# Performance work log

Measured on AMD Instinct MI355X. Metric: run time of the kernel, lower is better.

The kernel has to match this reference:

```python
import jax, jax.numpy as jnp
import numpy as np

IN_CH = 12
STEP = 4
UPLAG = 2048
HIDDEN = 1024
OUTPUT = 256
BATCH = 2048
FEAT = UPLAG // STEP  # per-channel conv output length


def setup_inputs() -> dict:
    key = jax.random.key(0)
    ks = jax.random.split(key, 7)
    s = 1.0 / np.sqrt(STEP)
    x = jax.random.normal(ks[0], (BATCH, IN_CH, UPLAG), dtype=jnp.float32)
    # per-channel Conv1d(1,1,step,step) weights/biases, stacked: [C, step], [C]
    W1 = jax.random.uniform(ks[1], (IN_CH, STEP), jnp.float32, -s, s)
    b1 = jax.random.uniform(ks[2], (IN_CH,), jnp.float32, -s, s)
    d_in = IN_CH * FEAT
    s2 = 1.0 / np.sqrt(d_in)
    W2 = jax.random.uniform(ks[3], (d_in, HIDDEN), jnp.float32, -s2, s2)
    b2 = jax.random.uniform(ks[4], (HIDDEN,), jnp.float32, -s2, s2)
    s3 = 1.0 / np.sqrt(HIDDEN)
    W3 = jax.random.uniform(ks[5], (HIDDEN, OUTPUT), jnp.float32, -s3, s3)
    b3 = jax.random.uniform(ks[6], (OUTPUT,), jnp.float32, -s3, s3)
    return {"x": x, "W1": W1, "b1": b1, "W2": W2, "b2": b2, "W3": W3, "b3": b3}


def reference(x, W1, b1, W2, b2, W3, b3):
    B, C, L = x.shape
    # Non-overlapping patch reduction equivalent to Conv1d(1,1,step,step) per channel:
    # view [B, C, F, step], contract step dim against per-channel kernel.
    xp = x.reshape(B, C, L // STEP, STEP)
    conv = jnp.einsum('bcfk,ck->bcf', xp, W1) + b1[None, :, None]  # [B, C, F]
    flat = conv.reshape(B, C * (L // STEP))  # concat order: channel-major, matches torch.cat
    h = jax.nn.relu(flat @ W2 + b2)
    out = h @ W3 + b3
    return out.reshape(B, 1, -1)
```

## Files before the change

kernel.cpp:

```cpp
#include <hip/hip_runtime.h>
#include <hip/hip_bf16.h>

#define BATCH   2048
#define IN_CH   12
#define UPLAG   2048
#define STEP    4
#define FEAT    512
#define DIN     6144
#define HIDDEN  1024
#define OUTPUT  256

typedef __bf16 bf16x8 __attribute__((ext_vector_type(8)));
typedef float  f32x4  __attribute__((ext_vector_type(4)));

__device__ __forceinline__ unsigned short f2bf(float f) {
  unsigned int u = __builtin_bit_cast(unsigned int, f);
  unsigned int r = (u + 0x7fffu + ((u >> 16) & 1u)) >> 16;
  return (unsigned short)r;
}

__device__ __forceinline__ float bf2f(unsigned short h) {
  unsigned int u = ((unsigned int)h) << 16;
  return __builtin_bit_cast(float, u);
}

__device__ __forceinline__ void async_copy16(const unsigned short* g, unsigned short* l) {
  __builtin_amdgcn_global_load_lds(
      (const __attribute__((address_space(1))) unsigned int*)g,
      (__attribute__((address_space(3))) unsigned int*)l, 16, 0, 0);
}

#define CONV_BLOCKS 4096
#define W2T_BLOCKS  1536
#define W3T_BLOCKS  64

__global__ __launch_bounds__(256) void prep_kernel(
    const float* __restrict__ x, const float* __restrict__ W1,
    const float* __restrict__ b1, unsigned short* __restrict__ flatA,
    const float* __restrict__ W2, unsigned short* __restrict__ W2T,
    const float* __restrict__ W3, unsigned short* __restrict__ W3T)
{
  __shared__ float tile[64][65];
  const int t = threadIdx.x;
  int b = blockIdx.x;

  if (b < CONV_BLOCKS) {
    const int total = BATCH * DIN;
    for (int gid = b * 256 + t; gid < total; gid += CONV_BLOCKS * 256) {
      int cf = gid % DIN;
      int c  = cf >> 9;
      float4 xv = ((const float4*)x)[gid];
      float4 wv = ((const float4*)W1)[c];
      float v = xv.x * wv.x + xv.y * wv.y + xv.z * wv.z + xv.w * wv.w + b1[c];
      flatA[gid] = f2bf(v);
    }
    return;
  }

  const float* in; unsigned short* outp; int R, Ncol, bx, by;
  if (b < CONV_BLOCKS + W2T_BLOCKS) {
    int idx = b - CONV_BLOCKS;
    in = W2; outp = W2T; R = DIN; Ncol = HIDDEN;
    bx = (idx & 15) * 64; by = (idx >> 4) * 64;
  } else {
    int idx = b - CONV_BLOCKS - W2T_BLOCKS;
    in = W3; outp = W3T; R = HIDDEN; Ncol = OUTPUT;
    bx = (idx & 3) * 64; by = (idx >> 2) * 64;
  }
  int tx = t & 63, ty = t >> 6;
  #pragma unroll
  for (int i = 0; i < 64; i += 4)
    tile[ty + i][tx] = in[(size_t)(by + ty + i) * Ncol + bx + tx];
  __syncthreads();
  #pragma unroll
  for (int i = 0; i < 64; i += 4)
    outp[(size_t)(bx + ty + i) * R + by + tx] = f2bf(tile[tx][ty + i]);
}

#define G1_BM 128
#define G1_BN 128
#define G1_BK 64
#define SPLITK 6

__global__ __launch_bounds__(256, 2) void gemm1_kernel(
    const unsigned short* __restrict__ A,
    const unsigned short* __restrict__ BT,
    unsigned short* __restrict__ Cp,
    int M, int N, int K)
{
  __shared__ unsigned short As[G1_BM * G1_BK];
  __shared__ unsigned short Bs[G1_BN * G1_BK];
  const int t    = threadIdx.x;
  const int lane = t & 63;
  const int wave = t >> 6;

  int b    = blockIdx.x;
  int xcdg = b & 7;
  int rest = b >> 3;
  int xt   = rest & 7;
  int zz   = rest >> 3;
  int zt   = zz >> 1;
  int yt   = (xcdg << 1) | (zz & 1);

  const int m0 = yt * G1_BM;
  const int n0 = xt * G1_BN;
  const int Ks = K / SPLITK;
  const int kbeg = zt * Ks;

  const int wm = (wave >> 1) * 64;
  const int wn = (wave & 1) * 64;
  const int lm = lane & 15;
  const int kgrp = lane >> 4;

  f32x4 acc[4][4];
  #pragma unroll
  for (int i = 0; i < 4; i++)
    #pragma unroll
    for (int j = 0; j < 4; j++) {
      f32x4 z = {0.f, 0.f, 0.f, 0.f};
      acc[i][j] = z;
    }

  const unsigned short* Ag = A  + (size_t)m0 * K + kbeg;
  const unsigned short* Bg = BT + (size_t)n0 * K + kbeg;

  for (int kk = 0; kk < Ks; kk += G1_BK) {
    #pragma unroll
    for (int r = 0; r < 4; ++r) {
      int c = r * 256 + t;
      int row = c >> 3;
      int gk  = (c & 7) ^ (row & 7);
      async_copy16(Ag + (size_t)row * K + kk + gk * 8, As + c * 8);
    }
    #pragma unroll
    for (int r = 0; r < 4; ++r) {
      int c = r * 256 + t;
      int row = c >> 3;
      int gk  = (c & 7) ^ (row & 7);
      async_copy16(Bg + (size_t)row * K + kk + gk * 8, Bs + c * 8);
    }
    __syncthreads();

    #pragma unroll
    for (int s = 0; s < 2; ++s) {
      const int kch = kgrp + s * 4;
      bf16x8 af[4], bfr[4];
      #pragma unroll
      for (int i = 0; i < 4; i++) {
        int row = wm + i * 16 + lm;
        af[i] = *(const bf16x8*)(As + row * G1_BK + ((kch ^ (row & 7)) * 8));
      }
      #pragma unroll
      for (int j = 0; j < 4; j++) {
        int row = wn + j * 16 + lm;
        bfr[j] = *(const bf16x8*)(Bs + row * G1_BK + ((kch ^ (row & 7)) * 8));
      }
      #pragma unroll
      for (int i = 0; i < 4; i++)
        #pragma unroll
        for (int j = 0; j < 4; j++)
          acc[i][j] = __builtin_amdgcn_mfma_f32_16x16x32_bf16(af[i], bfr[j], acc[i][j], 0, 0, 0);
    }
    __syncthreads();
  }

  unsigned short* Co = Cp + (size_t)zt * M * N;
  const int rbase = kgrp * 4;
  #pragma unroll
  for (int i = 0; i < 4; i++)
    #pragma unroll
    for (int j = 0; j < 4; j++) {
      int col = n0 + wn + j * 16 + lm;
      #pragma unroll
      for (int r = 0; r < 4; r++) {
        int row = m0 + wm + i * 16 + rbase + r;
        Co[(size_t)row * N + col] = f2bf(acc[i][j][r]);
      }
    }
}

__global__ __launch_bounds__(256) void reduce_bias_relu(
    const unsigned short* __restrict__ Cp, const float* __restrict__ b2,
    unsigned short* __restrict__ H)
{
  const int MN = BATCH * HIDDEN;
  int i4 = blockIdx.x * 256 + threadIdx.x;
  if (i4 >= MN / 4) return;
  float4 s = {0.f, 0.f, 0.f, 0.f};
  #pragma unroll
  for (int p = 0; p < SPLITK; ++p) {
    ushort4 a = ((const ushort4*)(Cp + (size_t)p * MN))[i4];
    s.x += bf2f(a.x); s.y += bf2f(a.y); s.z += bf2f(a.z); s.w += bf2f(a.w);
  }
  int col = (i4 * 4) & (HIDDEN - 1);
  float4 bb = *(const float4*)(b2 + col);
  ushort4 o;
  o.x = f2bf(fmaxf(s.x + bb.x, 0.f));
  o.y = f2bf(fmaxf(s.y + bb.y, 0.f));
  o.z = f2bf(fmaxf(s.z + bb.z, 0.f));
  o.w = f2bf(fmaxf(s.w + bb.w, 0.f));
  ((ushort4*)H)[i4] = o;
}

#define SPLITK2 4

__global__ __launch_bounds__(256, 2) void gemm2_kernel(
    const unsigned short* __restrict__ A,
    const unsigned short* __restrict__ BT,
    unsigned short* __restrict__ Cp)
{
  const int M = BATCH, N = OUTPUT, K = HIDDEN;
  __shared__ unsigned short As[64 * 64];
  __shared__ unsigned short Bs[64 * 64];
  const int t    = threadIdx.x;
  const int lane = t & 63;
  const int wave = t >> 6;
  const int m0 = blockIdx.y * 64;
  const int n0 = blockIdx.x * 64;
  const int Ks = K / SPLITK2;
  const int kbeg = blockIdx.z * Ks;
  const int wm = (wave >> 1) * 32;
  const int wn = (wave & 1) * 32;
  const int lm = lane & 15;
  const int kgrp = lane >> 4;

  f32x4 acc[2][2];
  #pragma unroll
  for (int i = 0; i < 2; i++)
    #pragma unroll
    for (int j = 0; j < 2; j++) {
      f32x4 z = {0.f, 0.f, 0.f, 0.f};
      acc[i][j] = z;
    }

  const unsigned short* Ag = A  + (size_t)m0 * K + kbeg;
  const unsigned short* Bg = BT + (size_t)n0 * K + kbeg;

  for (int kk = 0; kk < Ks; kk += 64) {
    #pragma unroll
    for (int r = 0; r < 2; ++r) {
      int c = r * 256 + t;
      int row = c >> 3;
      int gk  = (c & 7) ^ (row & 7);
      async_copy16(Ag + (size_t)row * K + kk + gk * 8, As + c * 8);
    }
    #pragma unroll
    for (int r = 0; r < 2; ++r) {
      int c = r * 256 + t;
      int row = c >> 3;
      int gk  = (c & 7) ^ (row & 7);
      async_copy16(Bg + (size_t)row * K + kk + gk * 8, Bs + c * 8);
    }
    __syncthreads();

    #pragma unroll
    for (int s = 0; s < 2; ++s) {
      const int kch = kgrp + s * 4;
      bf16x8 af[2], bfr[2];
      #pragma unroll
      for (int i = 0; i < 2; i++) {
        int row = wm + i * 16 + lm;
        af[i] = *(const bf16x8*)(As + row * 64 + ((kch ^ (row & 7)) * 8));
      }
      #pragma unroll
      for (int j = 0; j < 2; j++) {
        int row = wn + j * 16 + lm;
        bfr[j] = *(const bf16x8*)(Bs + row * 64 + ((kch ^ (row & 7)) * 8));
      }
      #pragma unroll
      for (int i = 0; i < 2; i++)
        #pragma unroll
        for (int j = 0; j < 2; j++)
          acc[i][j] = __builtin_amdgcn_mfma_f32_16x16x32_bf16(af[i], bfr[j], acc[i][j], 0, 0, 0);
    }
    __syncthreads();
  }

  unsigned short* Co = Cp + (size_t)blockIdx.z * M * N;
  const int rbase = kgrp * 4;
  #pragma unroll
  for (int i = 0; i < 2; i++)
    #pragma unroll
    for (int j = 0; j < 2; j++) {
      int col = n0 + wn + j * 16 + lm;
      #pragma unroll
      for (int r = 0; r < 4; r++) {
        int row_o = m0 + wm + i * 16 + rbase + r;
        Co[(size_t)row_o * N + col] = f2bf(acc[i][j][r]);
      }
    }
}

__global__ __launch_bounds__(256) void reduce2_bias(
    const unsigned short* __restrict__ Cp, const float* __restrict__ b3,
    float* __restrict__ out)
{
  const int MN = BATCH * OUTPUT;
  int i4 = blockIdx.x * 256 + threadIdx.x;
  if (i4 >= MN / 4) return;
  float4 s = {0.f, 0.f, 0.f, 0.f};
  #pragma unroll
  for (int p = 0; p < SPLITK2; ++p) {
    ushort4 a = ((const ushort4*)(Cp + (size_t)p * MN))[i4];
    s.x += bf2f(a.x); s.y += bf2f(a.y); s.z += bf2f(a.z); s.w += bf2f(a.w);
  }
  int col = (i4 * 4) & (OUTPUT - 1);
  float4 bb = *(const float4*)(b3 + col);
  float4 o = {s.x + bb.x, s.y + bb.y, s.z + bb.z, s.w + bb.w};
  ((float4*)out)[i4] = o;
}

extern "C" void kernel_launch(void* const* d_in, const int* in_sizes, int n_in,
                              void* d_out, int out_size, void* d_ws, size_t ws_size,
                              hipStream_t stream)
{
  const float* x  = (const float*)d_in[0];
  const float* W1 = (const float*)d_in[1];
  const float* b1 = (const float*)d_in[2];
  const float* W2 = (const float*)d_in[3];
  const float* b2 = (const float*)d_in[4];
  const float* W3 = (const float*)d_in[5];
  const float* b3 = (const float*)d_in[6];
  float* out = (float*)d_out;

  char* ws = (char*)d_ws;
  unsigned short* flatA = (unsigned short*)ws; ws += (size_t)BATCH * DIN * 2;
  unsigned short* W2T   = (unsigned short*)ws; ws += (size_t)HIDDEN * DIN * 2;
  unsigned short* W3T   = (unsigned short*)ws; ws += (size_t)OUTPUT * HIDDEN * 2;
  unsigned short* Cpart = (unsigned short*)ws; ws += (size_t)SPLITK * BATCH * HIDDEN * 2;
  unsigned short* H     = (unsigned short*)ws; ws += (size_t)BATCH * HIDDEN * 2;
  unsigned short* Cp2   = (unsigned short*)ws; ws += (size_t)SPLITK2 * BATCH * OUTPUT * 2;

  prep_kernel<<<CONV_BLOCKS + W2T_BLOCKS + W3T_BLOCKS, 256, 0, stream>>>(
      x, W1, b1, flatA, W2, W2T, W3, W3T);
  gemm1_kernel<<<768, 256, 0, stream>>>(flatA, W2T, Cpart, BATCH, HIDDEN, DIN);
  reduce_bias_relu<<<(BATCH * HIDDEN / 4) / 256, 256, 0, stream>>>(Cpart, b2, H);
  gemm2_kernel<<<dim3(OUTPUT / 64, BATCH / 64, SPLITK2), 256, 0, stream>>>(H, W3T, Cp2);
  reduce2_bias<<<(BATCH * OUTPUT / 4) / 256, 256, 0, stream>>>(Cp2, b3, out);
}
```

Measured before the change: 354.4 us.

## Fuse split-K reduce, bias+ReLU, second GEMM and output bias into one kernel

Replaces the three tail kernels (split-K reduction with bias+ReLU, split-K second GEMM, final reduction) with a single kernel. Each 16-row block reduces the gemm1 partials into a shared-memory H tile, then runs the 1024x256 GEMM directly with MFMA, adding b3 and writing fp32 output. This removes two launches and the round trips of H and the second partial buffer through global memory, and the second GEMM no longer goes through bf16 partials. In exchange, W3T is read from global memory without LDS staging by each of the 128 blocks, and the small M tile gives little reuse.

```diff
diff --git a/kernel.cpp b/kernel.cpp
--- a/kernel.cpp
+++ b/kernel.cpp
@@ -179,135 +179,75 @@
     }
 }
 
-__global__ __launch_bounds__(256) void reduce_bias_relu(
-    const unsigned short* __restrict__ Cp, const float* __restrict__ b2,
-    unsigned short* __restrict__ H)
-{
-  const int MN = BATCH * HIDDEN;
-  int i4 = blockIdx.x * 256 + threadIdx.x;
-  if (i4 >= MN / 4) return;
-  float4 s = {0.f, 0.f, 0.f, 0.f};
-  #pragma unroll
-  for (int p = 0; p < SPLITK; ++p) {
-    ushort4 a = ((const ushort4*)(Cp + (size_t)p * MN))[i4];
-    s.x += bf2f(a.x); s.y += bf2f(a.y); s.z += bf2f(a.z); s.w += bf2f(a.w);
-  }
-  int col = (i4 * 4) & (HIDDEN - 1);
-  float4 bb = *(const float4*)(b2 + col);
-  ushort4 o;
-  o.x = f2bf(fmaxf(s.x + bb.x, 0.f));
-  o.y = f2bf(fmaxf(s.y + bb.y, 0.f));
-  o.z = f2bf(fmaxf(s.z + bb.z, 0.f));
-  o.w = f2bf(fmaxf(s.w + bb.w, 0.f));
-  ((ushort4*)H)[i4] = o;
-}
-
-#define SPLITK2 4
-
-__global__ __launch_bounds__(256, 2) void gemm2_kernel(
-    const unsigned short* __restrict__ A,
-    const unsigned short* __restrict__ BT,
-    unsigned short* __restrict__ Cp)
-{
-  const int M = BATCH, N = OUTPUT, K = HIDDEN;
-  __shared__ unsigned short As[64 * 64];
-  __shared__ unsigned short Bs[64 * 64];
-  const int t    = threadIdx.x;
+#define TB_M 16
+#define HS_STRIDE (HIDDEN + 8)
+
+__global__ __launch_bounds__(256) void tail_kernel(
+    const unsigned short* __restrict__ Cp,
+    const float* __restrict__ b2,
+    const unsigned short* __restrict__ W3T,
+    const float* __restrict__ b3,
+    float* __restrict__ out)
+{
+  __shared__ unsigned short hs[TB_M * HS_STRIDE];
+  const int t = threadIdx.x;
   const int lane = t & 63;
   const int wave = t >> 6;
-  const int m0 = blockIdx.y * 64;
-  const int n0 = blockIdx.x * 64;
-  const int Ks = K / SPLITK2;
-  const int kbeg = blockIdx.z * Ks;
-  const int wm = (wave >> 1) * 32;
-  const int wn = (wave & 1) * 32;
+  const int m0 = blockIdx.x * TB_M;
+  const int MN = BATCH * HIDDEN;
+
+  for (int idx = t; idx < TB_M * (HIDDEN / 4); idx += 256) {
+    int r  = idx >> 8;
+    int c4 = idx & 255;
+    size_t base = (size_t)(m0 + r) * HIDDEN + c4 * 4;
+    float4 s = *(const float4*)(b2 + c4 * 4);
+    #pragma unroll
+    for (int p = 0; p < SPLITK; ++p) {
+      ushort4 a = *(const ushort4*)(Cp + (size_t)p * MN + base);
+      s.x += bf2f(a.x); s.y += bf2f(a.y); s.z += bf2f(a.z); s.w += bf2f(a.w);
+    }
+    ushort4 o;
+    o.x = f2bf(fmaxf(s.x, 0.f));
+    o.y = f2bf(fmaxf(s.y, 0.f));
+    o.z = f2bf(fmaxf(s.z, 0.f));
+    o.w = f2bf(fmaxf(s.w, 0.f));
+    *(ushort4*)(hs + r * HS_STRIDE + c4 * 4) = o;
+  }
+  __syncthreads();
+
   const int lm = lane & 15;
   const int kgrp = lane >> 4;
-
-  f32x4 acc[2][2];
-  #pragma unroll
-  for (int i = 0; i < 2; i++)
-    #pragma unroll
-    for (int j = 0; j < 2; j++) {
-      f32x4 z = {0.f, 0.f, 0.f, 0.f};
-      acc[i][j] = z;
-    }
-
-  const unsigned short* Ag = A  + (size_t)m0 * K + kbeg;
-  const unsigned short* Bg = BT + (size_t)n0 * K + kbeg;
-
-  for (int kk = 0; kk < Ks; kk += 64) {
-    #pragma unroll
-    for (int r = 0; r < 2; ++r) {
-      int c = r * 256 + t;
-      int row = c >> 3;
-      int gk  = (c & 7) ^ (row & 7);
-      async_copy16(Ag + (size_t)row * K + kk + gk * 8, As + c * 8);
-    }
-    #pragma unroll
-    for (int r = 0; r < 2; ++r) {
-      int c = r * 256 + t;
-      int row = c >> 3;
-      int gk  = (c & 7) ^ (row & 7);
-      async_copy16(Bg + (size_t)row * K + kk + gk * 8, Bs + c * 8);
-    }
-    __syncthreads();
-
-    #pragma unroll
-    for (int s = 0; s < 2; ++s) {
-      const int kch = kgrp + s * 4;
-      bf16x8 af[2], bfr[2];
-      #pragma unroll
-      for (int i = 0; i < 2; i++) {
-        int row = wm + i * 16 + lm;
-        af[i] = *(const bf16x8*)(As + row * 64 + ((kch ^ (row & 7)) * 8));
-      }
-      #pragma unroll
-      for (int j = 0; j < 2; j++) {
-        int row = wn + j * 16 + lm;
-        bfr[j] = *(const bf16x8*)(Bs + row * 64 + ((kch ^ (row & 7)) * 8));
-      }
-      #pragma unroll
-      for (int i = 0; i < 2; i++)
-        #pragma unroll
-        for (int j = 0; j < 2; j++)
-          acc[i][j] = __builtin_amdgcn_mfma_f32_16x16x32_bf16(af[i], bfr[j], acc[i][j], 0, 0, 0);
-    }
-    __syncthreads();
-  }
-
-  unsigned short* Co = Cp + (size_t)blockIdx.z * M * N;
+  const int ncol0 = wave * 64;
+  f32x4 acc[4];
+  #pragma unroll
+  for (int j = 0; j < 4; j++) {
+    f32x4 z = {0.f, 0.f, 0.f, 0.f};
+    acc[j] = z;
+  }
+
+  #pragma unroll 2
+  for (int kk = 0; kk < HIDDEN; kk += 32) {
+    bf16x8 af = *(const bf16x8*)(hs + lm * HS_STRIDE + kk + kgrp * 8);
+    #pragma unroll
+    for (int j = 0; j < 4; j++) {
+      const unsigned short* bp =
+          W3T + (size_t)(ncol0 + j * 16 + lm) * HIDDEN + kk + kgrp * 8;
+      bf16x8 bfr = *(const bf16x8*)bp;
+      acc[j] = __builtin_amdgcn_mfma_f32_16x16x32_bf16(af, bfr, acc[j], 0, 0, 0);
+    }
+  }
+
   const int rbase = kgrp * 4;
   #pragma unroll
-  for (int i = 0; i < 2; i++)
-    #pragma unroll
-    for (int j = 0; j < 2; j++) {
-      int col = n0 + wn + j * 16 + lm;
-      #pragma unroll
-      for (int r = 0; r < 4; r++) {
-        int row_o = m0 + wm + i * 16 + rbase + r;
-        Co[(size_t)row_o * N + col] = f2bf(acc[i][j][r]);
-      }
-    }
-}
-
-__global__ __launch_bounds__(256) void reduce2_bias(
-    const unsigned short* __restrict__ Cp, const float* __restrict__ b3,
-    float* __restrict__ out)
-{
-  const int MN = BATCH * OUTPUT;
-  int i4 = blockIdx.x * 256 + threadIdx.x;
-  if (i4 >= MN / 4) return;
-  float4 s = {0.f, 0.f, 0.f, 0.f};
-  #pragma unroll
-  for (int p = 0; p < SPLITK2; ++p) {
-    ushort4 a = ((const ushort4*)(Cp + (size_t)p * MN))[i4];
-    s.x += bf2f(a.x); s.y += bf2f(a.y); s.z += bf2f(a.z); s.w += bf2f(a.w);
-  }
-  int col = (i4 * 4) & (OUTPUT - 1);
-  float4 bb = *(const float4*)(b3 + col);
-  float4 o = {s.x + bb.x, s.y + bb.y, s.z + bb.z, s.w + bb.w};
-  ((float4*)out)[i4] = o;
+  for (int j = 0; j < 4; j++) {
+    int col = ncol0 + j * 16 + lm;
+    float bias = b3[col];
+    #pragma unroll
+    for (int r = 0; r < 4; r++) {
+      int row = m0 + rbase + r;
+      out[(size_t)row * OUTPUT + col] = acc[j][r] + bias;
+    }
+  }
 }
 
 extern "C" void kernel_launch(void* const* d_in, const int* in_sizes, int n_in,
@@ -328,13 +268,9 @@
   unsigned short* W2T   = (unsigned short*)ws; ws += (size_t)HIDDEN * DIN * 2;
   unsigned short* W3T   = (unsigned short*)ws; ws += (size_t)OUTPUT * HIDDEN * 2;
   unsigned short* Cpart = (unsigned short*)ws; ws += (size_t)SPLITK * BATCH * HIDDEN * 2;
-  unsigned short* H     = (unsigned short*)ws; ws += (size_t)BATCH * HIDDEN * 2;
-  unsigned short* Cp2   = (unsigned short*)ws; ws += (size_t)SPLITK2 * BATCH * OUTPUT * 2;
 
   prep_kernel<<<CONV_BLOCKS + W2T_BLOCKS + W3T_BLOCKS, 256, 0, stream>>>(
       x, W1, b1, flatA, W2, W2T, W3, W3T);
   gemm1_kernel<<<768, 256, 0, stream>>>(flatA, W2T, Cpart, BATCH, HIDDEN, DIN);
-  reduce_bias_relu<<<(BATCH * HIDDEN / 4) / 256, 256, 0, stream>>>(Cpart, b2, H);
-  gemm2_kernel<<<dim3(OUTPUT / 64, BATCH / 64, SPLITK2), 256, 0, stream>>>(H, W3T, Cp2);
-  reduce2_bias<<<(BATCH * OUTPUT / 4) / 256, 256, 0, stream>>>(Cp2, b3, out);
-}
+  tail_kernel<<<BATCH / TB_M, 256, 0, stream>>>(Cpart, b2, W3T, b3, out);
+}
```

After: 365.4 us. 3.1% more time.
